# Kernel optimization log

Measured on AMD Instinct MI355X. Metric: run time of the kernel, lower is better.

## Reference

```python
import jax, jax.numpy as jnp
import numpy as np

B, N, K, H, NC, NL = 512, 128, 16, 16, 6, 4  # batch, atoms, neighbors/atom, h_a, classes, EGNN layers

def _lin(key, fi, fo):
    lim = 1.0 / np.sqrt(fi)
    return jax.random.uniform(key, (fi, fo), jnp.float32, -lim, lim)

def _bias(key, fi, fo):
    lim = 1.0 / np.sqrt(fi)
    return jax.random.uniform(key, (fo,), jnp.float32, -lim, lim)

def setup_inputs():
    key = jax.random.key(0)
    kc, ke, ki, ko, kf, kl = jax.random.split(key, 6)
    coords = jax.random.normal(kc, (B, N, 3), dtype=jnp.float32)
    # fixed adjacency: node i -> (i+1 .. i+K) mod N, same for every frame
    adj = np.zeros((N, N), dtype=np.float32)
    idx = np.arange(N)
    for d in range(1, K + 1):
        adj[idx, (idx + d) % N] = 1.0
    data = jnp.concatenate([coords, jnp.broadcast_to(jnp.asarray(adj), (B, N, N))], axis=-1)  # [B,N,3+N]
    # edge-index construction (host-side; matches torch (edge_inds>0).nonzero().t(), row/col += offset*N)
    off, r, c = np.nonzero(np.broadcast_to(adj > 0.0, (B, N, N)))
    row = jnp.asarray(r + off * N, dtype=jnp.int32)
    col = jnp.asarray(c + off * N, dtype=jnp.int32)
    emb_w = jax.random.normal(ke, (N, H), dtype=jnp.float32)  # atom_emb.weight.data.normal_()
    k1, k2 = jax.random.split(ki); ein_w, ein_b = _lin(k1, H, H), _bias(k2, H, H)
    k1, k2 = jax.random.split(ko); eout_w, eout_b = _lin(k1, H, H), _bias(k2, H, H)
    k1, k2 = jax.random.split(kf); fc_w, fc_b = _lin(k1, H, NC), _bias(k2, H, NC)
    def make_layer(k):
        ks = jax.random.split(k, 11)
        xav = 0.001 * np.sqrt(6.0 / (H + 1))  # coord_mlp last layer: xavier_uniform gain=0.001, no bias
        return dict(
            e1_w=_lin(ks[0], 2 * H + 2, H), e1_b=_bias(ks[1], 2 * H + 2, H),
            e2_w=_lin(ks[2], H, H),        e2_b=_bias(ks[3], H, H),
            n1_w=_lin(ks[4], 2 * H, H),    n1_b=_bias(ks[5], 2 * H, H),
            n2_w=_lin(ks[6], H, H),        n2_b=_bias(ks[7], H, H),
            c1_w=_lin(ks[8], H, H),        c1_b=_bias(ks[9], H, H),
            c2_w=jax.random.uniform(ks[10], (H, 1), jnp.float32, -xav, xav))
    layers = [make_layer(k) for k in jax.random.split(kl, NL)]
    stacked = {name: jnp.stack([l[name] for l in layers]) for name in layers[0]}  # [NL, ...]
    out = dict(data=data, row=row, col=col, emb_w=emb_w, ein_w=ein_w, ein_b=ein_b,
               eout_w=eout_w, eout_b=eout_b, fc_w=fc_w, fc_b=fc_b)
    out.update(stacked)
    return out

def reference(data, row, col, emb_w, ein_w, ein_b, eout_w, eout_b, fc_w, fc_b,
              e1_w, e1_b, e2_w, e2_b, n1_w, n1_b, n2_w, n2_b, c1_w, c1_b, c2_w):
    Bn = data.shape[0] * data.shape[1]  # B*N flattened nodes
    silu = jax.nn.silu
    seg = lambda v: jax.ops.segment_sum(v, row, num_segments=Bn)
    # atom_emb(arange(N)) repeated over batch -> tile embedding table rows
    h = jnp.broadcast_to(emb_w[None, :, :], (data.shape[0], data.shape[1], H)).reshape(Bn, H)
    x = data[:, :, :3].reshape(Bn, 3).astype(jnp.float32)
    e_attr = jnp.ones((row.shape[0], 1), jnp.float32)
    cnt = jnp.maximum(seg(jnp.ones((row.shape[0],), jnp.float32)), 1.0)[:, None]  # for coords_agg='mean'
    h = h @ ein_w + ein_b  # embedding_in
    for l in range(NL):  # E_GCL layers (residual=True, attention=False)
        cd = x[row] - x[col]                                  # [E,3] coord_diff
        radial = jnp.sum(cd * cd, axis=1, keepdims=True)      # [E,1]
        ein = jnp.concatenate([h[row], h[col], radial, e_attr], axis=1)  # [E, 2H+2]
        m = silu(silu(ein @ e1_w[l] + e1_b[l]) @ e2_w[l] + e2_b[l])      # edge_mlp -> [E,H]
        t = silu(m @ c1_w[l] + c1_b[l]) @ c2_w[l]             # coord_mlp -> [E,1]
        x = x + seg(cd * t) / cnt                             # mean-aggregated coord update
        agg_m = seg(m)                                        # scatter-add messages to nodes
        h = h + (silu(jnp.concatenate([h, agg_m], axis=1) @ n1_w[l] + n1_b[l]) @ n2_w[l] + n2_b[l])
    h = h @ eout_w + eout_b  # embedding_out
    prot = jnp.sum(h.reshape(data.shape[0], data.shape[1], H), axis=1) / N  # pooling
    return jax.nn.softmax(prot @ fc_w + fc_b, axis=-1)
```

## Files before the change

kernel.cpp:

```cpp
#include <hip/hip_runtime.h>
#include <math.h>


#define NB   512
#define NN   128
#define HH   16
#define NCLS 6
#define NLAY 4
#define PAD  20

#define W_E1   0
#define W_E1B  544
#define W_E2   560
#define W_E2B  816
#define W_C1   832
#define W_C1B  1088
#define W_C2   1104
#define W_N1   1120
#define W_N1B  1632
#define W_N2   1648
#define W_N2B  1904
#define W_TOT  1920

__device__ __forceinline__ float silu_f(float v) {
    return __fdividef(v, 1.f + __expf(-v));
}

extern "C" __global__ __launch_bounds__(256)
void GraphVampNet_73624329388105_kernel(
    const float* __restrict__ data,
    const float* __restrict__ emb_w,
    const float* __restrict__ ein_w, const float* __restrict__ ein_b,
    const float* __restrict__ eout_w, const float* __restrict__ eout_b,
    const float* __restrict__ fc_w,  const float* __restrict__ fc_b,
    const float* __restrict__ e1_w,  const float* __restrict__ e1_b,
    const float* __restrict__ e2_w,  const float* __restrict__ e2_b,
    const float* __restrict__ n1_w,  const float* __restrict__ n1_b,
    const float* __restrict__ n2_w,  const float* __restrict__ n2_b,
    const float* __restrict__ c1_w,  const float* __restrict__ c1_b,
    const float* __restrict__ c2_w,
    float* __restrict__ out)
{
    __shared__ float h[NN][PAD];
    __shared__ float xs[NN][4];
    __shared__ float pA[NN][PAD];
    __shared__ float pB[NN][PAD];
    __shared__ float part[256][PAD];
    __shared__ __align__(16) float wb[W_TOT];
    __shared__ float hp[HH];
    __shared__ float prot[HH];

    const int b = blockIdx.x;
    const int t = threadIdx.x;

    if (t < NN) {
        const float* dp = data + ((size_t)b * NN + t) * (NN + 3);
        xs[t][0] = dp[0]; xs[t][1] = dp[1]; xs[t][2] = dp[2]; xs[t][3] = 0.f;

        float ev[HH];
        #pragma unroll
        for (int k = 0; k < HH; k++) ev[k] = emb_w[t * HH + k];
        float acc[HH];
        #pragma unroll
        for (int o = 0; o < HH; o++) acc[o] = ein_b[o];
        #pragma unroll
        for (int k = 0; k < HH; k++) {
            const float v = ev[k];
            #pragma unroll
            for (int o = 0; o < HH; o++) acc[o] += v * ein_w[k * HH + o];
        }
        #pragma unroll
        for (int o = 0; o < HH; o++) h[t][o] = acc[o];
    }

    for (int l = 0; l < NLAY; l++) {
        {
            const float* E1W = e1_w + l * 34 * HH;
            wb[W_E1 + t] = E1W[t];
            wb[W_E1 + 256 + t] = E1W[256 + t];
            if (t < 32) wb[W_E1 + 512 + t] = E1W[512 + t];
            wb[W_E2 + t] = e2_w[l * HH * HH + t];
            const float* N1W = n1_w + l * 2 * HH * HH;
            wb[W_N1 + t] = N1W[t];
            wb[W_N1 + 256 + t] = N1W[256 + t];
            wb[W_N2 + t] = n2_w[l * HH * HH + t];
            wb[W_C1 + t] = c1_w[l * HH * HH + t];
            if (t < HH) {
                wb[W_E1B + t] = e1_b[l * HH + t];
                wb[W_E2B + t] = e2_b[l * HH + t];
                wb[W_C1B + t] = c1_b[l * HH + t];
                wb[W_C2  + t] = c2_w[l * HH + t];
                wb[W_N1B + t] = n1_b[l * HH + t];
                wb[W_N2B + t] = n2_b[l * HH + t];
            }
        }
        __syncthreads();

        {
            const int node = t & (NN - 1);
            float hv[HH];
            #pragma unroll
            for (int k = 0; k < HH; k++) hv[k] = h[node][k];
            if (t < NN) {
                float acc[HH];
                #pragma unroll
                for (int o = 0; o < HH; o++) acc[o] = wb[W_E1B + o] + wb[W_E1 + 33 * HH + o];
                #pragma unroll
                for (int k = 0; k < HH; k++) {
                    const float v = hv[k];
                    #pragma unroll
                    for (int o = 0; o < HH; o++) acc[o] += v * wb[W_E1 + k * HH + o];
                }
                #pragma unroll
                for (int o = 0; o < HH; o++) pA[node][o] = acc[o];
            } else {
                float acc[HH];
                #pragma unroll
                for (int o = 0; o < HH; o++) acc[o] = 0.f;
                #pragma unroll
                for (int k = 0; k < HH; k++) {
                    const float v = hv[k];
                    #pragma unroll
                    for (int o = 0; o < HH; o++) acc[o] += v * wb[W_E1 + (16 + k) * HH + o];
                }
                #pragma unroll
                for (int o = 0; o < HH; o++) pB[node][o] = acc[o];
            }
        }
        __syncthreads();

        {
            const int i = t & (NN - 1);
            const int half = t >> 7;
            float pAi[HH];
            #pragma unroll
            for (int o = 0; o < HH; o++) pAi[o] = pA[i][o];
            const float4 xi = *(const float4*)&xs[i][0];
            float aggm[HH];
            #pragma unroll
            for (int o = 0; o < HH; o++) aggm[o] = 0.f;
            float cx0 = 0.f, cx1 = 0.f, cx2 = 0.f;

            #pragma unroll 1
            for (int g = 0; g < 4; g++) {
                unsigned o_col = W_E1 + 32 * HH;
                unsigned o_e2  = W_E2,  o_e2b = W_E2B;
                unsigned o_c1  = W_C1,  o_c1b = W_C1B;
                unsigned o_c2  = W_C2;
                asm volatile("" : "+v"(o_col), "+v"(o_e2), "+v"(o_e2b),
                                  "+v"(o_c1), "+v"(o_c1b), "+v"(o_c2));

                const int dbase = half * 8 + g * 2 + 1;
                const int j0 = (i + dbase) & (NN - 1);
                const int j1 = (i + dbase + 1) & (NN - 1);
                const float4 xj0 = *(const float4*)&xs[j0][0];
                const float4 xj1 = *(const float4*)&xs[j1][0];
                const float a00 = xi.x - xj0.x, a01 = xi.y - xj0.y, a02 = xi.z - xj0.z;
                const float a10 = xi.x - xj1.x, a11 = xi.y - xj1.y, a12 = xi.z - xj1.z;
                const float r0 = a00 * a00 + a01 * a01 + a02 * a02;
                const float r1 = a10 * a10 + a11 * a11 + a12 * a12;

                float m0[HH], m1v[HH];
                #pragma unroll
                for (int q = 0; q < 4; q++) {
                    const float4 wc  = ((const float4*)(wb + o_col))[q];
                    const float4 p0 = *(const float4*)&pB[j0][q * 4];
                    const float4 p1 = *(const float4*)&pB[j1][q * 4];
                    m0[q*4+0]  = silu_f(pAi[q*4+0] + p0.x + r0 * wc.x);
                    m0[q*4+1]  = silu_f(pAi[q*4+1] + p0.y + r0 * wc.y);
                    m0[q*4+2]  = silu_f(pAi[q*4+2] + p0.z + r0 * wc.z);
                    m0[q*4+3]  = silu_f(pAi[q*4+3] + p0.w + r0 * wc.w);
                    m1v[q*4+0] = silu_f(pAi[q*4+0] + p1.x + r1 * wc.x);
                    m1v[q*4+1] = silu_f(pAi[q*4+1] + p1.y + r1 * wc.y);
                    m1v[q*4+2] = silu_f(pAi[q*4+2] + p1.z + r1 * wc.z);
                    m1v[q*4+3] = silu_f(pAi[q*4+3] + p1.w + r1 * wc.w);
                }

                float ac0[HH], ac1[HH];
                #pragma unroll
                for (int q = 0; q < 4; q++) {
                    const float4 bb = ((const float4*)(wb + o_e2b))[q];
                    ac0[q*4+0] = bb.x; ac0[q*4+1] = bb.y; ac0[q*4+2] = bb.z; ac0[q*4+3] = bb.w;
                    ac1[q*4+0] = bb.x; ac1[q*4+1] = bb.y; ac1[q*4+2] = bb.z; ac1[q*4+3] = bb.w;
                }
                #pragma unroll
                for (int k = 0; k < HH; k++) {
                    const float v0 = m0[k], v1 = m1v[k];
                    #pragma unroll
                    for (int q = 0; q < 4; q++) {
                        const float4 w = ((const float4*)(wb + o_e2))[k * 4 + q];
                        ac0[q*4+0] += v0 * w.x; ac0[q*4+1] += v0 * w.y;
                        ac0[q*4+2] += v0 * w.z; ac0[q*4+3] += v0 * w.w;
                        ac1[q*4+0] += v1 * w.x; ac1[q*4+1] += v1 * w.y;
                        ac1[q*4+2] += v1 * w.z; ac1[q*4+3] += v1 * w.w;
                    }
                }
                #pragma unroll
                for (int o = 0; o < HH; o++) {
                    m0[o]  = silu_f(ac0[o]);
                    m1v[o] = silu_f(ac1[o]);
                    aggm[o] += m0[o] + m1v[o];
                }

                #pragma unroll
                for (int q = 0; q < 4; q++) {
                    const float4 bb = ((const float4*)(wb + o_c1b))[q];
                    ac0[q*4+0] = bb.x; ac0[q*4+1] = bb.y; ac0[q*4+2] = bb.z; ac0[q*4+3] = bb.w;
                    ac1[q*4+0] = bb.x; ac1[q*4+1] = bb.y; ac1[q*4+2] = bb.z; ac1[q*4+3] = bb.w;
                }
                #pragma unroll
                for (int k = 0; k < HH; k++) {
                    const float v0 = m0[k], v1 = m1v[k];
                    #pragma unroll
                    for (int q = 0; q < 4; q++) {
                        const float4 w = ((const float4*)(wb + o_c1))[k * 4 + q];
                        ac0[q*4+0] += v0 * w.x; ac0[q*4+1] += v0 * w.y;
                        ac0[q*4+2] += v0 * w.z; ac0[q*4+3] += v0 * w.w;
                        ac1[q*4+0] += v1 * w.x; ac1[q*4+1] += v1 * w.y;
                        ac1[q*4+2] += v1 * w.z; ac1[q*4+3] += v1 * w.w;
                    }
                }
                float t0 = 0.f, t1 = 0.f;
                #pragma unroll
                for (int q = 0; q < 4; q++) {
                    const float4 cw = ((const float4*)(wb + o_c2))[q];
                    t0 += silu_f(ac0[q*4+0]) * cw.x + silu_f(ac0[q*4+1]) * cw.y
                        + silu_f(ac0[q*4+2]) * cw.z + silu_f(ac0[q*4+3]) * cw.w;
                    t1 += silu_f(ac1[q*4+0]) * cw.x + silu_f(ac1[q*4+1]) * cw.y
                        + silu_f(ac1[q*4+2]) * cw.z + silu_f(ac1[q*4+3]) * cw.w;
                }

                cx0 += a00 * t0 + a10 * t1;
                cx1 += a01 * t0 + a11 * t1;
                cx2 += a02 * t0 + a12 * t1;
            }
            #pragma unroll
            for (int o = 0; o < HH; o++) part[t][o] = aggm[o];
            float4 cxv; cxv.x = cx0; cxv.y = cx1; cxv.z = cx2; cxv.w = 0.f;
            *(float4*)&part[t][16] = cxv;
        }
        __syncthreads();

        if (t < NN) {
            float aggm[HH];
            #pragma unroll
            for (int o = 0; o < HH; o++) aggm[o] = part[t][o] + part[t + NN][o];
            float hv[HH];
            #pragma unroll
            for (int k = 0; k < HH; k++) hv[k] = h[t][k];

            float acc[HH];
            #pragma unroll
            for (int o = 0; o < HH; o++) acc[o] = wb[W_N1B + o];
            #pragma unroll
            for (int k = 0; k < HH; k++) {
                const float v = hv[k];
                #pragma unroll
                for (int o = 0; o < HH; o++) acc[o] += v * wb[W_N1 + k * HH + o];
            }
            #pragma unroll
            for (int k = 0; k < HH; k++) {
                const float v = aggm[k];
                #pragma unroll
                for (int o = 0; o < HH; o++) acc[o] += v * wb[W_N1 + (16 + k) * HH + o];
            }
            float u[HH];
            #pragma unroll
            for (int o = 0; o < HH; o++) u[o] = silu_f(acc[o]);

            float acc2[HH];
            #pragma unroll
            for (int o = 0; o < HH; o++) acc2[o] = wb[W_N2B + o];
            #pragma unroll
            for (int k = 0; k < HH; k++) {
                const float v = u[k];
                #pragma unroll
                for (int o = 0; o < HH; o++) acc2[o] += v * wb[W_N2 + k * HH + o];
            }
            #pragma unroll
            for (int o = 0; o < HH; o++) h[t][o] = hv[o] + acc2[o];

            const float inv = 1.f / 16.f;
            xs[t][0] += (part[t][16] + part[t + NN][16]) * inv;
            xs[t][1] += (part[t][17] + part[t + NN][17]) * inv;
            xs[t][2] += (part[t][18] + part[t + NN][18]) * inv;
        }
        __syncthreads();
    }

    if (t < HH) {
        float acc = 0.f;
        for (int i = 0; i < NN; i++) acc += h[i][t];
        hp[t] = acc * (1.f / NN);
    }
    __syncthreads();
    if (t < HH) {
        float acc = eout_b[t];
        #pragma unroll
        for (int k = 0; k < HH; k++) acc += hp[k] * eout_w[k * HH + t];
        prot[t] = acc;
    }
    __syncthreads();
    if (t == 0) {
        float lg[NCLS];
        float mx = -1e30f;
        #pragma unroll
        for (int c = 0; c < NCLS; c++) {
            float acc = fc_b[c];
            #pragma unroll
            for (int k = 0; k < HH; k++) acc += prot[k] * fc_w[k * NCLS + c];
            lg[c] = acc;
            mx = fmaxf(mx, acc);
        }
        float s = 0.f;
        #pragma unroll
        for (int c = 0; c < NCLS; c++) { lg[c] = __expf(lg[c] - mx); s += lg[c]; }
        const float invs = 1.f / s;
        #pragma unroll
        for (int c = 0; c < NCLS; c++) out[b * NCLS + c] = lg[c] * invs;
    }
}

extern "C" void kernel_launch(void* const* d_in, const int* in_sizes, int n_in,
                              void* d_out, int out_size, void* d_ws, size_t ws_size,
                              hipStream_t stream) {
    const float* data   = (const float*)d_in[0];
    const float* emb_w  = (const float*)d_in[3];
    const float* ein_w  = (const float*)d_in[4];
    const float* ein_b  = (const float*)d_in[5];
    const float* eout_w = (const float*)d_in[6];
    const float* eout_b = (const float*)d_in[7];
    const float* fc_w   = (const float*)d_in[8];
    const float* fc_b   = (const float*)d_in[9];
    const float* e1_w   = (const float*)d_in[10];
    const float* e1_b   = (const float*)d_in[11];
    const float* e2_w   = (const float*)d_in[12];
    const float* e2_b   = (const float*)d_in[13];
    const float* n1_w   = (const float*)d_in[14];
    const float* n1_b   = (const float*)d_in[15];
    const float* n2_w   = (const float*)d_in[16];
    const float* n2_b   = (const float*)d_in[17];
    const float* c1_w   = (const float*)d_in[18];
    const float* c1_b   = (const float*)d_in[19];
    const float* c2_w   = (const float*)d_in[20];

    GraphVampNet_73624329388105_kernel<<<NB, 256, 0, stream>>>(
        data, emb_w, ein_w, ein_b, eout_w, eout_b, fc_w, fc_b,
        e1_w, e1_b, e2_w, e2_b, n1_w, n1_b, n2_w, n2_b, c1_w, c1_b, c2_w,
        (float*)d_out);
}
```

Baseline: 362.2 us.

## Double threads per block to split edge work four ways per node

```diff
diff --git a/kernel.cpp b/kernel.cpp
--- a/kernel.cpp
+++ b/kernel.cpp
@@ -26,7 +26,7 @@
     return __fdividef(v, 1.f + __expf(-v));
 }
 
-extern "C" __global__ __launch_bounds__(256)
+extern "C" __global__ __launch_bounds__(512, 4)
 void GraphVampNet_73624329388105_kernel(
     const float* __restrict__ data,
     const float* __restrict__ emb_w,
@@ -45,7 +45,7 @@
     __shared__ float xs[NN][4];
     __shared__ float pA[NN][PAD];
     __shared__ float pB[NN][PAD];
-    __shared__ float part[256][PAD];
+    __shared__ float part[3 * NN][PAD];
     __shared__ __align__(16) float wb[W_TOT];
     __shared__ float hp[HH];
     __shared__ float prot[HH];
@@ -77,14 +77,14 @@
         {
             const float* E1W = e1_w + l * 34 * HH;
             wb[W_E1 + t] = E1W[t];
-            wb[W_E1 + 256 + t] = E1W[256 + t];
             if (t < 32) wb[W_E1 + 512 + t] = E1W[512 + t];
-            wb[W_E2 + t] = e2_w[l * HH * HH + t];
             const float* N1W = n1_w + l * 2 * HH * HH;
             wb[W_N1 + t] = N1W[t];
-            wb[W_N1 + 256 + t] = N1W[256 + t];
-            wb[W_N2 + t] = n2_w[l * HH * HH + t];
-            wb[W_C1 + t] = c1_w[l * HH * HH + t];
+            if (t < 256) {
+                wb[W_E2 + t] = e2_w[l * HH * HH + t];
+                wb[W_C1 + t] = c1_w[l * HH * HH + t];
+                wb[W_N2 + t] = n2_w[l * HH * HH + t];
+            }
             if (t < HH) {
                 wb[W_E1B + t] = e1_b[l * HH + t];
                 wb[W_E2B + t] = e2_b[l * HH + t];
@@ -98,51 +98,54 @@
 
         {
             const int node = t & (NN - 1);
+            const int grp = t >> 7;
+            const int ob = (grp & 1) * 8;
             float hv[HH];
             #pragma unroll
             for (int k = 0; k < HH; k++) hv[k] = h[node][k];
-            if (t < NN) {
-                float acc[HH];
-                #pragma unroll
-                for (int o = 0; o < HH; o++) acc[o] = wb[W_E1B + o] + wb[W_E1 + 33 * HH + o];
+            if (grp < 2) {
+                float acc[8];
+                #pragma unroll
+                for (int o = 0; o < 8; o++)
+                    acc[o] = wb[W_E1B + ob + o] + wb[W_E1 + 33 * HH + ob + o];
                 #pragma unroll
                 for (int k = 0; k < HH; k++) {
                     const float v = hv[k];
                     #pragma unroll
-                    for (int o = 0; o < HH; o++) acc[o] += v * wb[W_E1 + k * HH + o];
-                }
-                #pragma unroll
-                for (int o = 0; o < HH; o++) pA[node][o] = acc[o];
+                    for (int o = 0; o < 8; o++) acc[o] += v * wb[W_E1 + k * HH + ob + o];
+                }
+                #pragma unroll
+                for (int o = 0; o < 8; o++) pA[node][ob + o] = acc[o];
             } else {
-                float acc[HH];
-                #pragma unroll
-                for (int o = 0; o < HH; o++) acc[o] = 0.f;
+                float acc[8];
+                #pragma unroll
+                for (int o = 0; o < 8; o++) acc[o] = 0.f;
                 #pragma unroll
                 for (int k = 0; k < HH; k++) {
                     const float v = hv[k];
                     #pragma unroll
-                    for (int o = 0; o < HH; o++) acc[o] += v * wb[W_E1 + (16 + k) * HH + o];
-                }
-                #pragma unroll
-                for (int o = 0; o < HH; o++) pB[node][o] = acc[o];
+                    for (int o = 0; o < 8; o++) acc[o] += v * wb[W_E1 + (16 + k) * HH + ob + o];
+                }
+                #pragma unroll
+                for (int o = 0; o < 8; o++) pB[node][ob + o] = acc[o];
             }
         }
         __syncthreads();
 
+        float aggm[HH];
+        float cx0 = 0.f, cx1 = 0.f, cx2 = 0.f;
         {
             const int i = t & (NN - 1);
-            const int half = t >> 7;
+            const int q4 = t >> 7;
             float pAi[HH];
             #pragma unroll
             for (int o = 0; o < HH; o++) pAi[o] = pA[i][o];
             const float4 xi = *(const float4*)&xs[i][0];
-            float aggm[HH];
             #pragma unroll
             for (int o = 0; o < HH; o++) aggm[o] = 0.f;
-            float cx0 = 0.f, cx1 = 0.f, cx2 = 0.f;
 
             #pragma unroll 1
-            for (int g = 0; g < 4; g++) {
+            for (int g = 0; g < 2; g++) {
                 unsigned o_col = W_E1 + 32 * HH;
                 unsigned o_e2  = W_E2,  o_e2b = W_E2B;
                 unsigned o_c1  = W_C1,  o_c1b = W_C1B;
@@ -150,7 +153,7 @@
                 asm volatile("" : "+v"(o_col), "+v"(o_e2), "+v"(o_e2b),
                                   "+v"(o_c1), "+v"(o_c1b), "+v"(o_c2));
 
-                const int dbase = half * 8 + g * 2 + 1;
+                const int dbase = q4 * 4 + g * 2 + 1;
                 const int j0 = (i + dbase) & (NN - 1);
                 const int j1 = (i + dbase + 1) & (NN - 1);
                 const float4 xj0 = *(const float4*)&xs[j0][0];
@@ -234,17 +237,20 @@
                 cx1 += a01 * t0 + a11 * t1;
                 cx2 += a02 * t0 + a12 * t1;
             }
-            #pragma unroll
-            for (int o = 0; o < HH; o++) part[t][o] = aggm[o];
-            float4 cxv; cxv.x = cx0; cxv.y = cx1; cxv.z = cx2; cxv.w = 0.f;
-            *(float4*)&part[t][16] = cxv;
+            if (t >= NN) {
+                #pragma unroll
+                for (int o = 0; o < HH; o++) part[t - NN][o] = aggm[o];
+                float4 cxv; cxv.x = cx0; cxv.y = cx1; cxv.z = cx2; cxv.w = 0.f;
+                *(float4*)&part[t - NN][16] = cxv;
+            }
         }
         __syncthreads();
 
         if (t < NN) {
-            float aggm[HH];
-            #pragma unroll
-            for (int o = 0; o < HH; o++) aggm[o] = part[t][o] + part[t + NN][o];
+            float am[HH];
+            #pragma unroll
+            for (int o = 0; o < HH; o++)
+                am[o] = aggm[o] + part[t][o] + part[t + NN][o] + part[t + 2 * NN][o];
             float hv[HH];
             #pragma unroll
             for (int k = 0; k < HH; k++) hv[k] = h[t][k];
@@ -260,7 +266,7 @@
             }
             #pragma unroll
             for (int k = 0; k < HH; k++) {
-                const float v = aggm[k];
+                const float v = am[k];
                 #pragma unroll
                 for (int o = 0; o < HH; o++) acc[o] += v * wb[W_N1 + (16 + k) * HH + o];
             }
@@ -281,9 +287,9 @@
             for (int o = 0; o < HH; o++) h[t][o] = hv[o] + acc2[o];
 
             const float inv = 1.f / 16.f;
-            xs[t][0] += (part[t][16] + part[t + NN][16]) * inv;
-            xs[t][1] += (part[t][17] + part[t + NN][17]) * inv;
-            xs[t][2] += (part[t][18] + part[t + NN][18]) * inv;
+            xs[t][0] += (cx0 + part[t][16] + part[t + NN][16] + part[t + 2 * NN][16]) * inv;
+            xs[t][1] += (cx1 + part[t][17] + part[t + NN][17] + part[t + 2 * NN][17]) * inv;
+            xs[t][2] += (cx2 + part[t][18] + part[t + NN][18] + part[t + 2 * NN][18]) * inv;
         }
         __syncthreads();
     }
@@ -344,7 +350,7 @@
     const float* c1_b   = (const float*)d_in[19];
     const float* c2_w   = (const float*)d_in[20];
 
-    GraphVampNet_73624329388105_kernel<<<NB, 256, 0, stream>>>(
+    GraphVampNet_73624329388105_kernel<<<NB, 512, 0, stream>>>(
         data, emb_w, ein_w, ein_b, eout_w, eout_b, fc_w, fc_b,
         e1_w, e1_b, e2_w, e2_b, n1_w, n1_b, n2_w, n2_b, c1_w, c1_b, c2_w,
         (float*)d_out);
```

Result: no change. 368.5 us (+1.7%).
